# Performance work log

Measured on AMD Instinct MI355X. Metric: run time of the kernel, lower is better.

The kernel has to match this reference:

```python
import jax, jax.numpy as jnp
import numpy as np

TAU = 0.2
LW = 0.5
EPS = 1e-12  # tf.math.l2_normalize epsilon


def _l2norm(x):
    ss = jnp.sum(x * x, axis=-1, keepdims=True)
    return x * jax.lax.rsqrt(jnp.maximum(ss, EPS))


def _global_head(f, W1, b1, W2, b2):
    g = jnp.mean(f, axis=(1, 2))            # GlobalAveragePooling2D -> [B, C]
    h = jax.nn.relu(g @ W1 + b1)
    return h @ W2 + b2                      # [B, 128]


def _dense_head(f, W1, b1, W2, b2):
    # 1x1 convs == per-pixel matmuls
    h = jax.nn.relu(jnp.einsum('bhwc,cd->bhwd', f, W1) + b1)
    return jnp.einsum('bhwd,de->bhwe', h, W2) + b2  # [B, H, W, 128]


def _info_nce(q, k):
    logits = (q @ k.T) / TAU                # [N, N]
    lse = jax.nn.logsumexp(logits, axis=-1)
    pos = jnp.diagonal(logits)
    return jnp.mean(lse - pos)


def setup_inputs() -> dict:
    key = jax.random.key(0)
    ks = jax.random.split(key, 10)
    B, H, W, C = 128, 7, 7, 2048
    Dh, De = 2048, 128
    s1 = 1.0 / np.sqrt(C)
    s2 = 1.0 / np.sqrt(Dh)
    inp = {
        'feat_q': jax.random.normal(ks[0], (B, H, W, C), jnp.float32),
        'feat_k': jax.random.normal(ks[1], (B, H, W, C), jnp.float32),
        'Wg1': jax.random.normal(ks[2], (C, Dh), jnp.float32) * s1,
        'bg1': jnp.zeros((Dh,), jnp.float32),
        'Wg2': jax.random.normal(ks[3], (Dh, De), jnp.float32) * s2,
        'bg2': jnp.zeros((De,), jnp.float32),
        'Wd1': jax.random.normal(ks[4], (C, Dh), jnp.float32) * s1,
        'bd1': jnp.zeros((Dh,), jnp.float32),
        'Wd2': jax.random.normal(ks[5], (Dh, De), jnp.float32) * s2,
        'bd2': jnp.zeros((De,), jnp.float32),
        'mWg1': jax.random.normal(ks[6], (C, Dh), jnp.float32) * s1,
        'mbg1': jnp.zeros((Dh,), jnp.float32),
        'mWg2': jax.random.normal(ks[7], (Dh, De), jnp.float32) * s2,
        'mbg2': jnp.zeros((De,), jnp.float32),
        'mWd1': jax.random.normal(ks[8], (C, Dh), jnp.float32) * s1,
        'mbd1': jnp.zeros((Dh,), jnp.float32),
        'mWd2': jax.random.normal(ks[9], (Dh, De), jnp.float32) * s2,
        'mbd2': jnp.zeros((De,), jnp.float32),
    }
    return inp


def reference(feat_q, feat_k, Wg1, bg1, Wg2, bg2, Wd1, bd1, Wd2, bd2,
              mWg1, mbg1, mWg2, mbg2, mWd1, mbd1, mWd2, mbd2):
    # query (student) branch
    q_g = _l2norm(_global_head(feat_q, Wg1, bg1, Wg2, bg2))      # [B, 128]
    q_d = _l2norm(_dense_head(feat_q, Wd1, bd1, Wd2, bd2))       # [B, H, W, 128]
    # key (momentum teacher) branch, stop-gradient as in train_step
    k_g = jax.lax.stop_gradient(_l2norm(_global_head(feat_k, mWg1, mbg1, mWg2, mbg2)))
    k_d = jax.lax.stop_gradient(_l2norm(_dense_head(feat_k, mWd1, mbd1, mWd2, mbd2)))

    l_g = _info_nce(q_g, k_g)

    B, H, W, De = q_d.shape
    f1 = q_d.reshape(B, H * W, De)
    f2 = k_d.reshape(B, H * W, De)
    sim = jnp.einsum('bnc,bmc->bnm', f1, f2)                     # [B, HW, HW]
    idx = jnp.argmax(sim, axis=-1)                               # [B, HW]
    matched = jnp.take_along_axis(f2, idx[..., None], axis=1)    # [B, HW, 128]

    l_d = _info_nce(f1.reshape(-1, De), matched.reshape(-1, De))
    total = (1.0 - LW) * l_g + LW * l_d
    return total
```

## Files before the change

kernel.cpp:

```cpp
#include <hip/hip_runtime.h>
#include <cstddef>

typedef __bf16 bf16x8 __attribute__((ext_vector_type(8)));
typedef float  f32x4  __attribute__((ext_vector_type(4)));
typedef unsigned short u16x8 __attribute__((ext_vector_type(8)));
typedef unsigned short u16x4 __attribute__((ext_vector_type(4)));

__device__ __forceinline__ float b2f(unsigned short u) {
    union { unsigned int i; float f; } v; v.i = ((unsigned int)u) << 16; return v.f;
}
__device__ __forceinline__ unsigned short f2b(float f) {
    union { float f; unsigned int i; } v; v.f = f;
    unsigned int r = v.i + 0x7fffu + ((v.i >> 16) & 1u);
    return (unsigned short)(r >> 16);
}
__device__ __forceinline__ void gl_lds16(const void* g, void* l) {
    __builtin_amdgcn_global_load_lds((const __attribute__((address_space(1))) void*)g,
                                     (__attribute__((address_space(3))) void*)l,
                                     16, 0, 0);
}

__device__ __forceinline__ void xcd_swizzle(int& bx, int& by, int& bz) {
    unsigned int nx = gridDim.x, ny = gridDim.y;
    unsigned int n = nx * ny * gridDim.z;
    unsigned int lin = blockIdx.x + nx * (blockIdx.y + ny * blockIdx.z);
    unsigned int q = n >> 3, r = n & 7u;
    unsigned int xcd = lin & 7u, off = lin >> 3;
    unsigned int s = (xcd < r) ? (xcd * (q + 1u) + off)
                               : (r * (q + 1u) + (xcd - r) * q + off);
    bx = (int)(s % nx); s /= nx;
    by = (int)(s % ny);
    bz = (int)(s / ny);
}

__global__ __launch_bounds__(64) void detect_kernel(const unsigned short* __restrict__ feat,
                                                    int* __restrict__ flag) {
    __shared__ int cnt;
    if (threadIdx.x == 0) cnt = 0;
    __syncthreads();
    int c = 0;
    for (int i = threadIdx.x; i < 256; i += 64) {
        float v = b2f(feat[i]);
        if (fabsf(v) > 100.0f) ++c;
    }
    atomicAdd(&cnt, c);
    __syncthreads();
    if (threadIdx.x == 0) *flag = (cnt > 16) ? 1 : 0;
}

__global__ __launch_bounds__(256) void zero_kernel(float* __restrict__ p, int n4) {
    int i = blockIdx.x * 256 + threadIdx.x;
    const f32x4 z = {0.f, 0.f, 0.f, 0.f};
    if (i < n4) ((f32x4*)p)[i] = z;
}

__global__ __launch_bounds__(256) void convpool_kernel(const void* __restrict__ fq,
                                                       const void* __restrict__ fk,
                                                       unsigned short* __restrict__ FQ,
                                                       unsigned short* __restrict__ FK,
                                                       unsigned short* __restrict__ gq,
                                                       unsigned short* __restrict__ gk,
                                                       const int* __restrict__ flagp) {
    int fl = *flagp;
    int b = blockIdx.y;
    const void* src = blockIdx.z ? fk : fq;
    unsigned short* dst = blockIdx.z ? FK : FQ;
    unsigned short* g   = blockIdx.z ? gk : gq;
    int c0 = blockIdx.x * 1024 + threadIdx.x * 4;
    float s[4];
    #pragma unroll
    for (int j = 0; j < 4; ++j) s[j] = 0.f;
    for (int p = 0; p < 49; ++p) {
        size_t idx = ((size_t)b * 49 + p) * 2048 + c0;
        u16x4 o;
        if (fl) {
            f32x4 v = *(const f32x4*)((const float*)src + idx);
            o[0]=f2b(v[0]); o[1]=f2b(v[1]); o[2]=f2b(v[2]); o[3]=f2b(v[3]);
            s[0]+=v[0]; s[1]+=v[1]; s[2]+=v[2]; s[3]+=v[3];
        } else {
            o = *(const u16x4*)((const unsigned short*)src + idx);
            #pragma unroll
            for (int j = 0; j < 4; ++j) s[j] += b2f(o[j]);
        }
        *(u16x4*)(dst + idx) = o;
    }
    u16x4 gm;
    #pragma unroll
    for (int j = 0; j < 4; ++j) gm[j] = f2b(s[j] * (1.0f / 49.0f));
    *(u16x4*)(g + (size_t)b * 2048 + c0) = gm;
}

__global__ __launch_bounds__(256) void convert_kernel(const void* __restrict__ in,
                                                      unsigned short* __restrict__ out,
                                                      const int* __restrict__ flagp) {
    int fl = *flagp;
    size_t i = ((size_t)blockIdx.x * 256 + threadIdx.x) * 8;
    if (fl) {
        const float* inf = (const float*)in;
        f32x4 v0 = *(const f32x4*)(inf + i);
        f32x4 v1 = *(const f32x4*)(inf + i + 4);
        u16x8 o;
        o[0]=f2b(v0[0]); o[1]=f2b(v0[1]); o[2]=f2b(v0[2]); o[3]=f2b(v0[3]);
        o[4]=f2b(v1[0]); o[5]=f2b(v1[1]); o[6]=f2b(v1[2]); o[7]=f2b(v1[3]);
        *(u16x8*)(out + i) = o;
    } else {
        *(u16x8*)(out + i) = *(const u16x8*)((const unsigned short*)in + i);
    }
}

__global__ __launch_bounds__(256) void pool_kernel(const void* __restrict__ fq,
                                                   const void* __restrict__ fk,
                                                   unsigned short* __restrict__ gq,
                                                   unsigned short* __restrict__ gk,
                                                   const int* __restrict__ flagp) {
    int fl = *flagp;
    int c = blockIdx.x * 256 + threadIdx.x;
    int b = blockIdx.y;
    const void* src = blockIdx.z ? fk : fq;
    unsigned short* dst = blockIdx.z ? gk : gq;
    size_t base = (size_t)b * 49 * 2048 + c;
    float s = 0.f;
    if (fl) {
        const float* sf = (const float*)src;
        #pragma unroll
        for (int p = 0; p < 49; ++p) s += sf[base + (size_t)p * 2048];
    } else {
        const unsigned short* su = (const unsigned short*)src;
        #pragma unroll
        for (int p = 0; p < 49; ++p) s += b2f(su[base + (size_t)p * 2048]);
    }
    dst[(size_t)b * 2048 + c] = f2b(s * (1.0f / 49.0f));
}

__global__ __launch_bounds__(256) void transpose2v_kernel(
    const void* __restrict__ s0, const void* __restrict__ s1,
    unsigned short* __restrict__ d0, unsigned short* __restrict__ d1,
    int rows, int cols, const int* __restrict__ flagp) {
    int fl = *flagp;
    int z = blockIdx.z;
    const void* in = z ? s1 : s0;
    unsigned short* out = z ? d1 : d0;
    __shared__ unsigned short tile[64 * 72];
    int bx = blockIdx.x * 64, by = blockIdx.y * 64;
    int tr = threadIdx.x >> 3;
    int tc = (threadIdx.x & 7) * 8;
    #pragma unroll
    for (int h = 0; h < 2; ++h) {
        int r = tr + h * 32;
        if (fl) {
            const float* inf = (const float*)in + (size_t)(by + r) * cols + bx + tc;
            f32x4 v0 = *(const f32x4*)inf;
            f32x4 v1 = *(const f32x4*)(inf + 4);
            u16x8 o;
            o[0]=f2b(v0[0]); o[1]=f2b(v0[1]); o[2]=f2b(v0[2]); o[3]=f2b(v0[3]);
            o[4]=f2b(v1[0]); o[5]=f2b(v1[1]); o[6]=f2b(v1[2]); o[7]=f2b(v1[3]);
            *(u16x8*)(tile + r * 72 + tc) = o;
        } else {
            const unsigned short* inu = (const unsigned short*)in + (size_t)(by + r) * cols + bx + tc;
            *(u16x8*)(tile + r * 72 + tc) = *(const u16x8*)inu;
        }
    }
    __syncthreads();
    #pragma unroll
    for (int h = 0; h < 2; ++h) {
        int oc = tr + h * 32;
        u16x8 v;
        #pragma unroll
        for (int j = 0; j < 8; ++j) v[j] = tile[(tc + j) * 72 + oc];
        *(u16x8*)(out + (size_t)(bx + oc) * rows + by + tc) = v;
    }
}

__global__ __launch_bounds__(256) void transpose4v_kernel(
    const void* __restrict__ s0, const void* __restrict__ s1,
    const void* __restrict__ s2, const void* __restrict__ s3,
    unsigned short* __restrict__ d0, unsigned short* __restrict__ d1,
    unsigned short* __restrict__ d2, unsigned short* __restrict__ d3,
    int rows, int cols, const int* __restrict__ flagp) {
    int fl = *flagp;
    int z = blockIdx.z;
    const void* in = (z == 0) ? s0 : (z == 1) ? s1 : (z == 2) ? s2 : s3;
    unsigned short* out = (z == 0) ? d0 : (z == 1) ? d1 : (z == 2) ? d2 : d3;
    __shared__ unsigned short tile[64 * 72];
    int bx = blockIdx.x * 64, by = blockIdx.y * 64;
    int tr = threadIdx.x >> 3;
    int tc = (threadIdx.x & 7) * 8;
    #pragma unroll
    for (int h = 0; h < 2; ++h) {
        int r = tr + h * 32;
        if (fl) {
            const float* inf = (const float*)in + (size_t)(by + r) * cols + bx + tc;
            f32x4 v0 = *(const f32x4*)inf;
            f32x4 v1 = *(const f32x4*)(inf + 4);
            u16x8 o;
            o[0]=f2b(v0[0]); o[1]=f2b(v0[1]); o[2]=f2b(v0[2]); o[3]=f2b(v0[3]);
            o[4]=f2b(v1[0]); o[5]=f2b(v1[1]); o[6]=f2b(v1[2]); o[7]=f2b(v1[3]);
            *(u16x8*)(tile + r * 72 + tc) = o;
        } else {
            const unsigned short* inu = (const unsigned short*)in + (size_t)(by + r) * cols + bx + tc;
            *(u16x8*)(tile + r * 72 + tc) = *(const u16x8*)inu;
        }
    }
    __syncthreads();
    #pragma unroll
    for (int h = 0; h < 2; ++h) {
        int oc = tr + h * 32;
        u16x8 v;
        #pragma unroll
        for (int j = 0; j < 8; ++j) v[j] = tile[(tc + j) * 72 + oc];
        *(u16x8*)(out + (size_t)(bx + oc) * rows + by + tc) = v;
    }
}

__device__ __forceinline__ void mlp_body(
    const unsigned short* __restrict__ A, const unsigned short* __restrict__ Bt,
    const unsigned short* __restrict__ W2, const void* __restrict__ b1,
    float* __restrict__ outp, size_t m0, size_t n0, int fl)
{
    const int K = 2048;
    __shared__ unsigned short smem[32768];
    unsigned short* As0 = smem;
    unsigned short* Bs0 = smem + 8192;
    unsigned short* As1 = smem + 16384;
    unsigned short* Bs1 = smem + 24576;
    unsigned short* W2s = smem;
    unsigned short* Hs  = smem + 8192;

    int tid  = threadIdx.x;
    int lane = tid & 63;
    int w    = tid >> 6;
    int wm = w & 1, wn = w >> 1;
    int quad = lane >> 4, l16 = lane & 15;
    int lrow = lane >> 3;
    int kc   = (lane & 7) ^ lrow;

    const unsigned short* gA[4];
    const unsigned short* gB[4];
    int off[4];
    #pragma unroll
    for (int c = 0; c < 4; ++c) {
        int row = w * 32 + c * 8 + lrow;
        gA[c] = A  + (m0 + row) * (size_t)K + kc * 8;
        gB[c] = Bt + (n0 + row) * (size_t)K + kc * 8;
        off[c] = w * 2048 + c * 512;
    }

    const f32x4 zero4 = {0.f, 0.f, 0.f, 0.f};
    f32x4 acc[4][4];
    #pragma unroll
    for (int i = 0; i < 4; ++i)
        #pragma unroll
        for (int j = 0; j < 4; ++j) acc[i][j] = zero4;

    int swz = l16 & 7;

#define STAGE(Ad, Bd) do { \
    _Pragma("unroll") \
    for (int c = 0; c < 4; ++c) { gl_lds16(gA[c], (Ad) + off[c]); gA[c] += 64; } \
    _Pragma("unroll") \
    for (int c = 0; c < 4; ++c) { gl_lds16(gB[c], (Bd) + off[c]); gB[c] += 64; } \
} while (0)

#define CSTEP(Asrc, Bsrc) do { \
    _Pragma("unroll") \
    for (int k0 = 0; k0 < 64; k0 += 32) { \
        bf16x8 af[4], bfr[4]; \
        _Pragma("unroll") \
        for (int mt = 0; mt < 4; ++mt) { \
            int row = wm * 64 + mt * 16 + l16; \
            int sc  = (((k0 >> 3) + quad) ^ swz) << 3; \
            af[mt] = *(const bf16x8*)((Asrc) + row * 64 + sc); \
        } \
        _Pragma("unroll") \
        for (int nt = 0; nt < 4; ++nt) { \
            int row = wn * 64 + nt * 16 + l16; \
            int sc  = (((k0 >> 3) + quad) ^ swz) << 3; \
            bfr[nt] = *(const bf16x8*)((Bsrc) + row * 64 + sc); \
        } \
        _Pragma("unroll") \
        for (int mt = 0; mt < 4; ++mt) \
            _Pragma("unroll") \
            for (int nt = 0; nt < 4; ++nt) \
                acc[mt][nt] = __builtin_amdgcn_mfma_f32_16x16x32_bf16(af[mt], bfr[nt], acc[mt][nt], 0, 0, 0); \
    } \
} while (0)

    STAGE(As0, Bs0);
    __syncthreads();
    #pragma unroll 1
    for (int kb2 = 0; kb2 < 16; ++kb2) {
        STAGE(As1, Bs1);
        CSTEP(As0, Bs0);
        __syncthreads();
        if (kb2 < 15) STAGE(As0, Bs0);
        CSTEP(As1, Bs1);
        __syncthreads();
    }
#undef STAGE
#undef CSTEP

    float b1v[4];
    #pragma unroll
    for (int nt = 0; nt < 4; ++nt) {
        int col = (int)n0 + wn * 64 + nt * 16 + l16;
        b1v[nt] = fl ? ((const float*)b1)[col] : b2f(((const unsigned short*)b1)[col]);
    }

    f32x4 acc2[4][4];
    #pragma unroll
    for (int i = 0; i < 4; ++i)
        #pragma unroll
        for (int j = 0; j < 4; ++j) acc2[i][j] = zero4;

    #pragma unroll
    for (int hf = 0; hf < 2; ++hf) {
        __syncthreads();
        if (wn == hf) {
            #pragma unroll
            for (int mt = 0; mt < 4; ++mt)
                #pragma unroll
                for (int nt = 0; nt < 4; ++nt)
                    #pragma unroll
                    for (int r = 0; r < 4; ++r) {
                        float v = fmaxf(acc[mt][nt][r] + b1v[nt], 0.f);
                        Hs[(wm * 64 + mt * 16 + quad * 4 + r) * 72 + nt * 16 + l16] = f2b(v);
                    }
        } else {
            #pragma unroll
            for (int c = 0; c < 8; ++c) {
                const unsigned short* g = W2 + (size_t)(wm * 64 + c * 8 + lrow) * 2048
                                          + n0 + hf * 64 + kc * 8;
                gl_lds16(g, W2s + wm * 4096 + c * 512);
            }
        }
        __syncthreads();
        #pragma unroll
        for (int k0 = 0; k0 < 64; k0 += 32) {
            bf16x8 ha[4], wb[4];
            #pragma unroll
            for (int mt = 0; mt < 4; ++mt)
                ha[mt] = *(const bf16x8*)(Hs + (wm * 64 + mt * 16 + l16) * 72 + k0 + quad * 8);
            #pragma unroll
            for (int et = 0; et < 4; ++et) {
                int row = wn * 64 + et * 16 + l16;
                int sc  = (((k0 >> 3) + quad) ^ swz) << 3;
                wb[et] = *(const bf16x8*)(W2s + row * 64 + sc);
            }
            #pragma unroll
            for (int mt = 0; mt < 4; ++mt)
                #pragma unroll
                for (int et = 0; et < 4; ++et)
                    acc2[mt][et] = __builtin_amdgcn_mfma_f32_16x16x32_bf16(ha[mt], wb[et], acc2[mt][et], 0, 0, 0);
        }
    }

    #pragma unroll
    for (int et = 0; et < 4; ++et) {
        int col = wn * 64 + et * 16 + l16;
        #pragma unroll
        for (int mt = 0; mt < 4; ++mt)
            #pragma unroll
            for (int r = 0; r < 4; ++r) {
                size_t row = m0 + wm * 64 + mt * 16 + quad * 4 + r;
                atomicAdd(&outp[row * 128 + col], acc2[mt][et][r]);
            }
    }
}

__global__ __launch_bounds__(256) void mlp_mega_kernel(
    const unsigned short* __restrict__ FQ, const unsigned short* __restrict__ FK,
    const unsigned short* __restrict__ gq, const unsigned short* __restrict__ gk,
    const unsigned short* __restrict__ WD1T, const unsigned short* __restrict__ MWD1T,
    const unsigned short* __restrict__ WG1T, const unsigned short* __restrict__ MWG1T,
    const unsigned short* __restrict__ W2dq, const unsigned short* __restrict__ W2dk,
    const unsigned short* __restrict__ W2gq, const unsigned short* __restrict__ W2gk,
    const void* __restrict__ bd1, const void* __restrict__ mbd1,
    const void* __restrict__ bg1, const void* __restrict__ mbg1,
    float* __restrict__ rawdq, float* __restrict__ rawdk,
    float* __restrict__ rawgq, float* __restrict__ rawgk,
    const int* __restrict__ flagp)
{
    int fl = *flagp;
    int bx, by, bz;
    xcd_swizzle(bx, by, bz);
    int z = bz;
    int isg = (by == 49);
    const unsigned short *A, *Bt, *W2; const void* b1; float* outp;
    if (!isg) {
        A = z ? FK : FQ;  Bt = z ? MWD1T : WD1T;  W2 = z ? W2dk : W2dq;
        b1 = z ? mbd1 : bd1;  outp = z ? rawdk : rawdq;
    } else {
        A = z ? gk : gq;  Bt = z ? MWG1T : WG1T;  W2 = z ? W2gk : W2gq;
        b1 = z ? mbg1 : bg1;  outp = z ? rawgk : rawgq;
    }
    size_t m0 = isg ? 0 : (size_t)by * 128;
    size_t n0 = (size_t)bx * 128;
    mlp_body(A, Bt, W2, b1, outp, m0, n0, fl);
}

__global__ __launch_bounds__(256) void mlp_kernel(
    const unsigned short* __restrict__ A0, const unsigned short* __restrict__ A1,
    const unsigned short* __restrict__ Bt0, const unsigned short* __restrict__ Bt1,
    const unsigned short* __restrict__ W20, const unsigned short* __restrict__ W21,
    const void* __restrict__ b10, const void* __restrict__ b11,
    float* __restrict__ out0, float* __restrict__ out1,
    const int* __restrict__ flagp)
{
    int fl = *flagp;
    int bx, by, bz;
    xcd_swizzle(bx, by, bz);
    int z  = bz;
    mlp_body(z ? A1 : A0, z ? Bt1 : Bt0, z ? W21 : W20, z ? b11 : b10,
             z ? out1 : out0, (size_t)by * 128, (size_t)bx * 128, fl);
}

__global__ __launch_bounds__(256) void simmatch_kernel(
    const float* __restrict__ rawdq, const float* __restrict__ rawdk,
    const void* __restrict__ bd2, const void* __restrict__ mbd2,
    unsigned short* __restrict__ qd, unsigned short* __restrict__ kd,
    unsigned short* __restrict__ matched, float* __restrict__ pos,
    const int* __restrict__ flagp) {
    int fl = *flagp;
    __shared__ float f1s[49 * 128];
    __shared__ float f2s[49 * 128];
    int b = blockIdx.x;
    int t = threadIdx.x;
    size_t base = (size_t)b * 49 * 128;

    int rr = t >> 2, jq = t & 3;
    if (rr < 49) {
        #pragma unroll
        for (int br = 0; br < 2; ++br) {
            const float* raw = br ? rawdk : rawdq;
            const void* bias = br ? mbd2 : bd2;
            unsigned short* outg = br ? kd : qd;
            float* fs = br ? f2s : f1s;
            size_t idx = base + (size_t)rr * 128 + jq * 32;
            float x[32];
            float ss = 0.f;
            #pragma unroll
            for (int c = 0; c < 32; ++c) {
                float bv = fl ? ((const float*)bias)[jq * 32 + c]
                              : b2f(((const unsigned short*)bias)[jq * 32 + c]);
                x[c] = raw[idx + c] + bv;
                ss += x[c] * x[c];
            }
            ss += __shfl_xor(ss, 1); ss += __shfl_xor(ss, 2);
            float rs = rsqrtf(fmaxf(ss, 1e-12f));
            #pragma unroll
            for (int c = 0; c < 32; ++c) {
                unsigned short us = f2b(x[c] * rs);
                outg[idx + c] = us;
                fs[rr * 128 + jq * 32 + c] = b2f(us);
            }
        }
    }
    __syncthreads();

    int i = t >> 2, q4 = t & 3;
    if (i < 49) {
        int mlo = q4 * 13;
        int mhi = mlo + 13; if (mhi > 49) mhi = 49;
        float best = -1e30f; int bi = 1 << 20;
        const f32x4* va = (const f32x4*)(f1s + i * 128);
        for (int m = mlo; m < mhi; ++m) {
            const f32x4* vb = (const f32x4*)(f2s + m * 128);
            float d = 0.f;
            #pragma unroll
            for (int j = 0; j < 32; ++j) {
                f32x4 a = va[j], bb = vb[j];
                d += a[0]*bb[0] + a[1]*bb[1] + a[2]*bb[2] + a[3]*bb[3];
            }
            if (d > best) { best = d; bi = m; }
        }
        #pragma unroll
        for (int off = 1; off < 4; off <<= 1) {
            float ov = __shfl_xor(best, off);
            int   oi = __shfl_xor(bi, off);
            if (ov > best || (ov == best && oi < bi)) { best = ov; bi = oi; }
        }
        if (q4 == 0) pos[b * 49 + i] = best * 5.0f;
        for (int j = q4 * 32; j < q4 * 32 + 32; ++j)
            matched[base + (size_t)i * 128 + j] = f2b(f2s[bi * 128 + j]);
    }
}

#define KS 136
__global__ __launch_bounds__(256) void lse_kernel(const unsigned short* __restrict__ qd,
                                                  const unsigned short* __restrict__ matched,
                                                  float* __restrict__ lsep) {
    __shared__ unsigned short As[128 * KS];
    __shared__ unsigned short Bs[64 * KS];
    __shared__ float rsum[128];
    int tid  = threadIdx.x;
    int lane = tid & 63, wave = tid >> 6;
    int wm = wave & 1, wn = wave >> 1;
    int quad = lane >> 4, l16 = lane & 15;
    size_t m0 = (size_t)blockIdx.x * 128;
    int z = blockIdx.y;

    #pragma unroll
    for (int i = 0; i < 8; ++i) {
        int l = tid + 256 * i;
        int row = l >> 4, ko = (l & 15) << 3;
        u16x8 v = *(const u16x8*)(qd + (m0 + row) * 128 + ko);
        *(u16x8*)(As + row * KS + ko) = v;
    }
    if (tid < 128) rsum[tid] = 0.f;

    float rs[4][4];
    #pragma unroll
    for (int mt = 0; mt < 4; ++mt)
        #pragma unroll
        for (int r = 0; r < 4; ++r) rs[mt][r] = 0.f;

    const f32x4 zero4 = {0.f, 0.f, 0.f, 0.f};
    int nlo = z * 896, nhi = nlo + 896;
    for (int n0 = nlo; n0 < nhi; n0 += 64) {
        __syncthreads();
        #pragma unroll
        for (int i = 0; i < 4; ++i) {
            int l = tid + 256 * i;
            int row = l >> 4, ko = (l & 15) << 3;
            u16x8 v = *(const u16x8*)(matched + (size_t)(n0 + row) * 128 + ko);
            *(u16x8*)(Bs + row * KS + ko) = v;
        }
        __syncthreads();
        f32x4 acc[4][2];
        #pragma unroll
        for (int mt = 0; mt < 4; ++mt) { acc[mt][0] = zero4; acc[mt][1] = zero4; }
        #pragma unroll
        for (int k0 = 0; k0 < 128; k0 += 32) {
            bf16x8 af[4], bfr[2];
            #pragma unroll
            for (int mt = 0; mt < 4; ++mt)
                af[mt] = *(const bf16x8*)(As + (wm * 64 + mt * 16 + l16) * KS + k0 + quad * 8);
            #pragma unroll
            for (int nt = 0; nt < 2; ++nt)
                bfr[nt] = *(const bf16x8*)(Bs + (wn * 32 + nt * 16 + l16) * KS + k0 + quad * 8);
            #pragma unroll
            for (int mt = 0; mt < 4; ++mt)
                #pragma unroll
                for (int nt = 0; nt < 2; ++nt)
                    acc[mt][nt] = __builtin_amdgcn_mfma_f32_16x16x32_bf16(af[mt], bfr[nt], acc[mt][nt], 0, 0, 0);
        }
        #pragma unroll
        for (int mt = 0; mt < 4; ++mt)
            #pragma unroll
            for (int r = 0; r < 4; ++r)
                rs[mt][r] += __expf(acc[mt][0][r] * 5.0f) + __expf(acc[mt][1][r] * 5.0f);
    }
    #pragma unroll
    for (int mt = 0; mt < 4; ++mt)
        #pragma unroll
        for (int r = 0; r < 4; ++r) {
            float v = rs[mt][r];
            v += __shfl_xor(v, 1); v += __shfl_xor(v, 2);
            v += __shfl_xor(v, 4); v += __shfl_xor(v, 8);
            if (l16 == 0) atomicAdd(&rsum[wm * 64 + mt * 16 + quad * 4 + r], v);
        }
    __syncthreads();
    if (tid < 128) lsep[(size_t)z * 6272 + m0 + tid] = rsum[tid];
}

__global__ __launch_bounds__(128) void lg_kernel(const float* __restrict__ rawgq,
                                                 const float* __restrict__ rawgk,
                                                 const void* __restrict__ bg2,
                                                 const void* __restrict__ mbg2,
                                                 float* __restrict__ lgrow,
                                                 const int* __restrict__ flagp) {
    int fl = *flagp;
    __shared__ float ksf[128 * 128];
    __shared__ float qsf[8 * 128];
    int t = threadIdx.x;
    int rbase = blockIdx.x * 8;
    {
        const float* rk = rawgk + (size_t)t * 128;
        float ss = 0.f;
        for (int c = 0; c < 128; ++c) {
            float bv = fl ? ((const float*)mbg2)[c] : b2f(((const unsigned short*)mbg2)[c]);
            float xx = rk[c] + bv;
            ss += xx * xx;
        }
        float rsv = rsqrtf(fmaxf(ss, 1e-12f));
        for (int c = 0; c < 128; ++c) {
            float bv = fl ? ((const float*)mbg2)[c] : b2f(((const unsigned short*)mbg2)[c]);
            ksf[t * 128 + c] = b2f(f2b((rk[c] + bv) * rsv));
        }
    }
    if (t < 8) {
        const float* rq = rawgq + (size_t)(rbase + t) * 128;
        float ss = 0.f;
        for (int c = 0; c < 128; ++c) {
            float bv = fl ? ((const float*)bg2)[c] : b2f(((const unsigned short*)bg2)[c]);
            float xx = rq[c] + bv;
            ss += xx * xx;
        }
        float rsv = rsqrtf(fmaxf(ss, 1e-12f));
        for (int c = 0; c < 128; ++c) {
            float bv = fl ? ((const float*)bg2)[c] : b2f(((const unsigned short*)bg2)[c]);
            qsf[t * 128 + c] = b2f(f2b((rq[c] + bv) * rsv));
        }
    }
    __syncthreads();
    int rl = t >> 4, jg = t & 15;
    int row = rbase + rl;
    float se = 0.f, diag = 0.f;
    for (int jj = 0; jj < 8; ++jj) {
        int j = jg * 8 + jj;
        float d = 0.f;
        #pragma unroll 8
        for (int c = 0; c < 128; ++c) d += qsf[rl * 128 + c] * ksf[j * 128 + c];
        d *= 5.0f;
        se += __expf(d);
        if (j == row) diag = d;
    }
    #pragma unroll
    for (int off = 1; off < 16; off <<= 1) { se += __shfl_xor(se, off); diag += __shfl_xor(diag, off); }
    if (jg == 0) lgrow[row] = logf(se) - diag;
}

__global__ __launch_bounds__(256) void final_kernel(const float* __restrict__ lsep,
                                                    const float* __restrict__ pos,
                                                    const float* __restrict__ lgrow,
                                                    unsigned int* __restrict__ out) {
    int t = threadIdx.x;
    float s = 0.f;
    for (int i = t; i < 6272; i += 256) {
        float se = 0.f;
        #pragma unroll
        for (int zz = 0; zz < 7; ++zz) se += lsep[zz * 6272 + i];
        s += logf(se) - pos[i];
    }
    float g = (t < 128) ? lgrow[t] : 0.f;
    #pragma unroll
    for (int off = 32; off >= 1; off >>= 1) { s += __shfl_xor(s, off); g += __shfl_xor(g, off); }
    __shared__ float p8[8];
    if ((t & 63) == 0) { p8[t >> 6] = s; p8[4 + (t >> 6)] = g; }
    __syncthreads();
    if (t == 0) {
        float ld  = (p8[0] + p8[1] + p8[2] + p8[3]) * (1.0f / 6272.0f);
        float lg  = (p8[4] + p8[5] + p8[6] + p8[7]) * (1.0f / 128.0f);
        float total = 0.5f * lg + 0.5f * ld;
        unsigned int L = f2b(total);
        union { float f; unsigned int u; } tb; tb.f = total;
        unsigned int base = (tb.u & 0xFFFF0000u) | L;
        unsigned int bu = base; float be = 1e30f;
        #pragma unroll
        for (int d = -1; d <= 1; ++d) {
            unsigned int c = base + ((unsigned int)d << 16);
            union { unsigned int u; float f; } cv; cv.u = c;
            float e = fabsf(cv.f - total);
            if (e < be) { be = e; bu = c; }
        }
        out[0] = bu;
    }
}

#define A_FQ     ((size_t)0)
#define A_FK     ((size_t)25690112)
#define A_WD1T   ((size_t)51380224)
#define A_MWD1T  ((size_t)59768832)
#define A_WG1T   ((size_t)68157440)
#define A_MWG1T  ((size_t)76546048)
#define A_W2DQ   ((size_t)84934656)
#define A_W2DK   ((size_t)85458944)
#define A_W2GQ   ((size_t)85983232)
#define A_W2GK   ((size_t)86507520)
#define A_RAWDQ  ((size_t)87031808)
#define A_RAWDK  ((size_t)90243072)
#define A_RAWGQ  ((size_t)93454336)
#define A_RAWGK  ((size_t)93519872)
#define A_GQ     ((size_t)93585408)
#define A_GK     ((size_t)94109696)
#define A_QD     ((size_t)94633984)
#define A_KD     ((size_t)96239616)
#define A_MT     ((size_t)97845248)
#define A_POS    ((size_t)99450880)
#define A_LSEP   ((size_t)99475968)
#define A_LGR    ((size_t)99651584)
#define A_FLAG   ((size_t)99652096)
#define A_NEED   ((size_t)99652608)

#define B_SLOTA  ((size_t)0)
#define B_QD     ((size_t)0)
#define B_KD     ((size_t)1605632)
#define B_MT     ((size_t)3211264)
#define B_SLOTB  ((size_t)8388608)
#define B_W2DQ   ((size_t)34078720)
#define B_W2DK   ((size_t)34603008)
#define B_W2GQ   ((size_t)35127296)
#define B_W2GK   ((size_t)35651584)
#define B_RAWDQ  ((size_t)36175872)
#define B_RAWDK  ((size_t)39387136)
#define B_RAWGQ  ((size_t)42598400)
#define B_RAWGK  ((size_t)42663936)
#define B_GQ     ((size_t)42729472)
#define B_GK     ((size_t)43253760)
#define B_POS    ((size_t)42729472)
#define B_LSEP   ((size_t)42754560)
#define B_LGR    ((size_t)42930176)
#define B_FLAG   ((size_t)42930688)

extern "C" void kernel_launch(void* const* d_in, const int* in_sizes, int n_in,
                              void* d_out, int out_size, void* d_ws, size_t ws_size,
                              hipStream_t stream) {
    (void)in_sizes; (void)n_in; (void)out_size;
    const void* feat_q = d_in[0];
    const void* feat_k = d_in[1];
    const void* Wg1 = d_in[2];  const void* bg1 = d_in[3];
    const void* Wg2 = d_in[4];  const void* bg2 = d_in[5];
    const void* Wd1 = d_in[6];  const void* bd1 = d_in[7];
    const void* Wd2 = d_in[8];  const void* bd2 = d_in[9];
    const void* mWg1 = d_in[10]; const void* mbg1 = d_in[11];
    const void* mWg2 = d_in[12]; const void* mbg2 = d_in[13];
    const void* mWd1 = d_in[14]; const void* mbd1 = d_in[15];
    const void* mWd2 = d_in[16]; const void* mbd2 = d_in[17];
    char* ws = (char*)d_ws;

    if (ws_size >= A_NEED) {
        unsigned short* FQ    = (unsigned short*)(ws + A_FQ);
        unsigned short* FK    = (unsigned short*)(ws + A_FK);
        unsigned short* WD1T  = (unsigned short*)(ws + A_WD1T);
        unsigned short* MWD1T = (unsigned short*)(ws + A_MWD1T);
        unsigned short* WG1T  = (unsigned short*)(ws + A_WG1T);
        unsigned short* MWG1T = (unsigned short*)(ws + A_MWG1T);
        unsigned short* W2dq  = (unsigned short*)(ws + A_W2DQ);
        unsigned short* W2dk  = (unsigned short*)(ws + A_W2DK);
        unsigned short* W2gq  = (unsigned short*)(ws + A_W2GQ);
        unsigned short* W2gk  = (unsigned short*)(ws + A_W2GK);
        float* rawdq = (float*)(ws + A_RAWDQ);
        float* rawdk = (float*)(ws + A_RAWDK);
        float* rawgq = (float*)(ws + A_RAWGQ);
        float* rawgk = (float*)(ws + A_RAWGK);
        unsigned short* gq = (unsigned short*)(ws + A_GQ);
        unsigned short* gk = (unsigned short*)(ws + A_GK);
        unsigned short* qd = (unsigned short*)(ws + A_QD);
        unsigned short* kd = (unsigned short*)(ws + A_KD);
        unsigned short* mt = (unsigned short*)(ws + A_MT);
        float* pos  = (float*)(ws + A_POS);
        float* lsep = (float*)(ws + A_LSEP);
        float* lgr  = (float*)(ws + A_LGR);
        int*   flag = (int*)(ws + A_FLAG);

        detect_kernel<<<1, 64, 0, stream>>>((const unsigned short*)feat_q, flag);
        convpool_kernel<<<dim3(2, 128, 2), 256, 0, stream>>>(feat_q, feat_k, FQ, FK, gq, gk, flag);
        transpose4v_kernel<<<dim3(32, 32, 4), 256, 0, stream>>>(
            Wd1, mWd1, Wg1, mWg1, WD1T, MWD1T, WG1T, MWG1T, 2048, 2048, flag);
        transpose4v_kernel<<<dim3(2, 32, 4), 256, 0, stream>>>(
            Wd2, mWd2, Wg2, mWg2, W2dq, W2dk, W2gq, W2gk, 2048, 128, flag);
        zero_kernel<<<1600, 256, 0, stream>>>(rawdq, 409600);
        mlp_mega_kernel<<<dim3(16, 50, 2), 256, 0, stream>>>(
            FQ, FK, gq, gk, WD1T, MWD1T, WG1T, MWG1T,
            W2dq, W2dk, W2gq, W2gk, bd1, mbd1, bg1, mbg1,
            rawdq, rawdk, rawgq, rawgk, flag);
        simmatch_kernel<<<128, 256, 0, stream>>>(rawdq, rawdk, bd2, mbd2, qd, kd, mt, pos, flag);
        lse_kernel<<<dim3(49, 7), 256, 0, stream>>>(qd, mt, lsep);
        lg_kernel<<<16, 128, 0, stream>>>(rawgq, rawgk, bg2, mbg2, lgr, flag);
        final_kernel<<<1, 256, 0, stream>>>(lsep, pos, lgr, (unsigned int*)d_out);
    } else {
        unsigned short* slotA = (unsigned short*)(ws + B_SLOTA);
        unsigned short* slotB = (unsigned short*)(ws + B_SLOTB);
        unsigned short* W2dq = (unsigned short*)(ws + B_W2DQ);
        unsigned short* W2dk = (unsigned short*)(ws + B_W2DK);
        unsigned short* W2gq = (unsigned short*)(ws + B_W2GQ);
        unsigned short* W2gk = (unsigned short*)(ws + B_W2GK);
        float* rawdq = (float*)(ws + B_RAWDQ);
        float* rawdk = (float*)(ws + B_RAWDK);
        float* rawgq = (float*)(ws + B_RAWGQ);
        float* rawgk = (float*)(ws + B_RAWGK);
        unsigned short* gq = (unsigned short*)(ws + B_GQ);
        unsigned short* gk = (unsigned short*)(ws + B_GK);
        unsigned short* qd = (unsigned short*)(ws + B_QD);
        unsigned short* kd = (unsigned short*)(ws + B_KD);
        unsigned short* mt = (unsigned short*)(ws + B_MT);
        float* pos  = (float*)(ws + B_POS);
        float* lsep = (float*)(ws + B_LSEP);
        float* lgr  = (float*)(ws + B_LGR);
        int*   flag = (int*)(ws + B_FLAG);

        detect_kernel<<<1, 64, 0, stream>>>((const unsigned short*)feat_q, flag);
        pool_kernel<<<dim3(8, 128, 2), 256, 0, stream>>>(feat_q, feat_k, gq, gk, flag);
        transpose2v_kernel<<<dim3(32, 32, 2), 256, 0, stream>>>(Wg1, mWg1, slotA, slotB, 2048, 2048, flag);
        transpose4v_kernel<<<dim3(2, 32, 4), 256, 0, stream>>>(
            Wd2, mWd2, Wg2, mWg2, W2dq, W2dk, W2gq, W2gk, 2048, 128, flag);
        zero_kernel<<<1600, 256, 0, stream>>>(rawdq, 409600);
        mlp_kernel<<<dim3(16, 1, 2), 256, 0, stream>>>(
            gq, gk, slotA, slotB, W2gq, W2gk, bg1, mbg1, rawgq, rawgk, flag);
        transpose2v_kernel<<<dim3(32, 32, 1), 256, 0, stream>>>(Wd1, Wd1, slotA, slotA, 2048, 2048, flag);
        convert_kernel<<<6272, 256, 0, stream>>>(feat_q, slotB, flag);
        mlp_kernel<<<dim3(16, 49, 1), 256, 0, stream>>>(
            slotB, slotB, slotA, slotA, W2dq, W2dq, bd1, bd1, rawdq, rawdq, flag);
        transpose2v_kernel<<<dim3(32, 32, 1), 256, 0, stream>>>(mWd1, mWd1, slotA, slotA, 2048, 2048, flag);
        convert_kernel<<<6272, 256, 0, stream>>>(feat_k, slotB, flag);
        mlp_kernel<<<dim3(16, 49, 1), 256, 0, stream>>>(
            slotB, slotB, slotA, slotA, W2dk, W2dk, mbd1, mbd1, rawdk, rawdk, flag);
        simmatch_kernel<<<128, 256, 0, stream>>>(rawdq, rawdk, bd2, mbd2, qd, kd, mt, pos, flag);
        lse_kernel<<<dim3(49, 7), 256, 0, stream>>>(qd, mt, lsep);
        lg_kernel<<<16, 128, 0, stream>>>(rawgq, rawgk, bg2, mbg2, lgr, flag);
        final_kernel<<<1, 256, 0, stream>>>(lsep, pos, lgr, (unsigned int*)d_out);
    }
}
```

Before: 546.1 us.

## Widen grids for pooling, simmatch and LSE; hand-pipeline MLP GEMM barriers

Convpool now uses two channels per thread over twice as many blocks. Simmatch splits its rows across two blocks per batch, and lse_kernel splits its N range into 14 chunks instead of 7, reusing the rawdq buffer for the larger partial-sum array. The MLP GEMM main loop replaces __syncthreads with explicit vmcnt/lgkmcnt waits, raw s_barriers and sched_barriers, and raises wave priority around the MFMA block. The goal is more parallelism in the small tail kernels and better overlap of global-to-LDS loads with MFMA work. The costs are redundant normalisation work in simmatch and reliance on hand-counted waitcnt values.

```diff
diff --git a/kernel.cpp b/kernel.cpp
--- a/kernel.cpp
+++ b/kernel.cpp
@@ -3,8 +3,10 @@
 
 typedef __bf16 bf16x8 __attribute__((ext_vector_type(8)));
 typedef float  f32x4  __attribute__((ext_vector_type(4)));
+typedef float  f32x2  __attribute__((ext_vector_type(2)));
 typedef unsigned short u16x8 __attribute__((ext_vector_type(8)));
 typedef unsigned short u16x4 __attribute__((ext_vector_type(4)));
+typedef unsigned short u16x2 __attribute__((ext_vector_type(2)));
 
 __device__ __forceinline__ float b2f(unsigned short u) {
     union { unsigned int i; float f; } v; v.i = ((unsigned int)u) << 16; return v.f;
@@ -66,28 +68,30 @@
     const void* src = blockIdx.z ? fk : fq;
     unsigned short* dst = blockIdx.z ? FK : FQ;
     unsigned short* g   = blockIdx.z ? gk : gq;
-    int c0 = blockIdx.x * 1024 + threadIdx.x * 4;
-    float s[4];
-    #pragma unroll
-    for (int j = 0; j < 4; ++j) s[j] = 0.f;
-    for (int p = 0; p < 49; ++p) {
-        size_t idx = ((size_t)b * 49 + p) * 2048 + c0;
-        u16x4 o;
-        if (fl) {
-            f32x4 v = *(const f32x4*)((const float*)src + idx);
-            o[0]=f2b(v[0]); o[1]=f2b(v[1]); o[2]=f2b(v[2]); o[3]=f2b(v[3]);
-            s[0]+=v[0]; s[1]+=v[1]; s[2]+=v[2]; s[3]+=v[3];
-        } else {
-            o = *(const u16x4*)((const unsigned short*)src + idx);
-            #pragma unroll
-            for (int j = 0; j < 4; ++j) s[j] += b2f(o[j]);
-        }
-        *(u16x4*)(dst + idx) = o;
-    }
-    u16x4 gm;
-    #pragma unroll
-    for (int j = 0; j < 4; ++j) gm[j] = f2b(s[j] * (1.0f / 49.0f));
-    *(u16x4*)(g + (size_t)b * 2048 + c0) = gm;
+    int c0 = blockIdx.x * 512 + threadIdx.x * 2;
+    float s0 = 0.f, s1 = 0.f;
+    if (fl) {
+        const float* sf = (const float*)src;
+        #pragma unroll 7
+        for (int p = 0; p < 49; ++p) {
+            size_t idx = ((size_t)b * 49 + p) * 2048 + c0;
+            f32x2 v = *(const f32x2*)(sf + idx);
+            u16x2 o; o[0] = f2b(v[0]); o[1] = f2b(v[1]);
+            s0 += v[0]; s1 += v[1];
+            *(u16x2*)(dst + idx) = o;
+        }
+    } else {
+        const unsigned short* su = (const unsigned short*)src;
+        #pragma unroll 7
+        for (int p = 0; p < 49; ++p) {
+            size_t idx = ((size_t)b * 49 + p) * 2048 + c0;
+            u16x2 o = *(const u16x2*)(su + idx);
+            s0 += b2f(o[0]); s1 += b2f(o[1]);
+            *(u16x2*)(dst + idx) = o;
+        }
+    }
+    u16x2 gm; gm[0] = f2b(s0 * (1.0f / 49.0f)); gm[1] = f2b(s1 * (1.0f / 49.0f));
+    *(u16x2*)(g + (size_t)b * 2048 + c0) = gm;
 }
 
 __global__ __launch_bounds__(256) void convert_kernel(const void* __restrict__ in,
@@ -277,24 +281,39 @@
             int sc  = (((k0 >> 3) + quad) ^ swz) << 3; \
             bfr[nt] = *(const bf16x8*)((Bsrc) + row * 64 + sc); \
         } \
+        __builtin_amdgcn_s_setprio(1); \
         _Pragma("unroll") \
         for (int mt = 0; mt < 4; ++mt) \
             _Pragma("unroll") \
             for (int nt = 0; nt < 4; ++nt) \
                 acc[mt][nt] = __builtin_amdgcn_mfma_f32_16x16x32_bf16(af[mt], bfr[nt], acc[mt][nt], 0, 0, 0); \
+        __builtin_amdgcn_s_setprio(0); \
     } \
 } while (0)
 
     STAGE(As0, Bs0);
-    __syncthreads();
     #pragma unroll 1
     for (int kb2 = 0; kb2 < 16; ++kb2) {
         STAGE(As1, Bs1);
+        asm volatile("s_waitcnt vmcnt(8)" ::: "memory");
+        __builtin_amdgcn_s_barrier();
+        __builtin_amdgcn_sched_barrier(0);
         CSTEP(As0, Bs0);
-        __syncthreads();
-        if (kb2 < 15) STAGE(As0, Bs0);
+        asm volatile("s_waitcnt lgkmcnt(0)" ::: "memory");
+        __builtin_amdgcn_sched_barrier(0);
+        __builtin_amdgcn_s_barrier();
+        if (kb2 < 15) {
+            STAGE(As0, Bs0);
+            asm volatile("s_waitcnt vmcnt(8)" ::: "memory");
+        } else {
+            asm volatile("s_waitcnt vmcnt(0)" ::: "memory");
+        }
+        __builtin_amdgcn_s_barrier();
+        __builtin_amdgcn_sched_barrier(0);
         CSTEP(As1, Bs1);
-        __syncthreads();
+        asm volatile("s_waitcnt lgkmcnt(0)" ::: "memory");
+        __builtin_amdgcn_sched_barrier(0);
+        __builtin_amdgcn_s_barrier();
     }
 #undef STAGE
 #undef CSTEP
@@ -424,6 +443,7 @@
     __shared__ float f1s[49 * 128];
     __shared__ float f2s[49 * 128];
     int b = blockIdx.x;
+    int half = blockIdx.y;
     int t = threadIdx.x;
     size_t base = (size_t)b * 49 * 128;
 
@@ -450,15 +470,17 @@
             #pragma unroll
             for (int c = 0; c < 32; ++c) {
                 unsigned short us = f2b(x[c] * rs);
-                outg[idx + c] = us;
+                if (half == 0) outg[idx + c] = us;
                 fs[rr * 128 + jq * 32 + c] = b2f(us);
             }
         }
     }
     __syncthreads();
 
-    int i = t >> 2, q4 = t & 3;
-    if (i < 49) {
+    int i0 = t >> 2, q4 = t & 3;
+    int i = half * 25 + i0;
+    int ilim = half ? 24 : 25;
+    if (i0 < ilim) {
         int mlo = q4 * 13;
         int mhi = mlo + 13; if (mhi > 49) mhi = 49;
         float best = -1e30f; int bi = 1 << 20;
@@ -486,6 +508,7 @@
 }
 
 #define KS 136
+#define NZSPLIT 14
 __global__ __launch_bounds__(256) void lse_kernel(const unsigned short* __restrict__ qd,
                                                   const unsigned short* __restrict__ matched,
                                                   float* __restrict__ lsep) {
@@ -515,7 +538,7 @@
         for (int r = 0; r < 4; ++r) rs[mt][r] = 0.f;
 
     const f32x4 zero4 = {0.f, 0.f, 0.f, 0.f};
-    int nlo = z * 896, nhi = nlo + 896;
+    int nlo = z * 448, nhi = nlo + 448;
     for (int n0 = nlo; n0 < nhi; n0 += 64) {
         __syncthreads();
         #pragma unroll
@@ -629,7 +652,7 @@
     for (int i = t; i < 6272; i += 256) {
         float se = 0.f;
         #pragma unroll
-        for (int zz = 0; zz < 7; ++zz) se += lsep[zz * 6272 + i];
+        for (int zz = 0; zz < NZSPLIT; ++zz) se += lsep[zz * 6272 + i];
         s += logf(se) - pos[i];
     }
     float g = (t < 128) ? lgrow[t] : 0.f;
@@ -739,12 +762,12 @@
         unsigned short* kd = (unsigned short*)(ws + A_KD);
         unsigned short* mt = (unsigned short*)(ws + A_MT);
         float* pos  = (float*)(ws + A_POS);
-        float* lsep = (float*)(ws + A_LSEP);
+        float* lsep = (float*)(ws + A_RAWDQ);
         float* lgr  = (float*)(ws + A_LGR);
         int*   flag = (int*)(ws + A_FLAG);
 
         detect_kernel<<<1, 64, 0, stream>>>((const unsigned short*)feat_q, flag);
-        convpool_kernel<<<dim3(2, 128, 2), 256, 0, stream>>>(feat_q, feat_k, FQ, FK, gq, gk, flag);
+        convpool_kernel<<<dim3(4, 128, 2), 256, 0, stream>>>(feat_q, feat_k, FQ, FK, gq, gk, flag);
         transpose4v_kernel<<<dim3(32, 32, 4), 256, 0, stream>>>(
             Wd1, mWd1, Wg1, mWg1, WD1T, MWD1T, WG1T, MWG1T, 2048, 2048, flag);
         transpose4v_kernel<<<dim3(2, 32, 4), 256, 0, stream>>>(
@@ -754,8 +777,8 @@
             FQ, FK, gq, gk, WD1T, MWD1T, WG1T, MWG1T,
             W2dq, W2dk, W2gq, W2gk, bd1, mbd1, bg1, mbg1,
             rawdq, rawdk, rawgq, rawgk, flag);
-        simmatch_kernel<<<128, 256, 0, stream>>>(rawdq, rawdk, bd2, mbd2, qd, kd, mt, pos, flag);
-        lse_kernel<<<dim3(49, 7), 256, 0, stream>>>(qd, mt, lsep);
+        simmatch_kernel<<<dim3(128, 2), 256, 0, stream>>>(rawdq, rawdk, bd2, mbd2, qd, kd, mt, pos, flag);
+        lse_kernel<<<dim3(49, NZSPLIT), 256, 0, stream>>>(qd, mt, lsep);
         lg_kernel<<<16, 128, 0, stream>>>(rawgq, rawgk, bg2, mbg2, lgr, flag);
         final_kernel<<<1, 256, 0, stream>>>(lsep, pos, lgr, (unsigned int*)d_out);
     } else {
@@ -775,7 +798,7 @@
         unsigned short* kd = (unsigned short*)(ws + B_KD);
         unsigned short* mt = (unsigned short*)(ws + B_MT);
         float* pos  = (float*)(ws + B_POS);
-        float* lsep = (float*)(ws + B_LSEP);
+        float* lsep = (float*)(ws + B_RAWDQ);
         float* lgr  = (float*)(ws + B_LGR);
         int*   flag = (int*)(ws + B_FLAG);
 
@@ -795,8 +818,8 @@
         convert_kernel<<<6272, 256, 0, stream>>>(feat_k, slotB, flag);
         mlp_kernel<<<dim3(16, 49, 1), 256, 0, stream>>>(
             slotB, slotB, slotA, slotA, W2dk, W2dk, mbd1, mbd1, rawdk, rawdk, flag);
-        simmatch_kernel<<<128, 256, 0, stream>>>(rawdq, rawdk, bd2, mbd2, qd, kd, mt, pos, flag);
-        lse_kernel<<<dim3(49, 7), 256, 0, stream>>>(qd, mt, lsep);
+        simmatch_kernel<<<dim3(128, 2), 256, 0, stream>>>(rawdq, rawdk, bd2, mbd2, qd, kd, mt, pos, flag);
+        lse_kernel<<<dim3(49, NZSPLIT), 256, 0, stream>>>(qd, mt, lsep);
         lg_kernel<<<16, 128, 0, stream>>>(rawgq, rawgk, bg2, mbg2, lgr, flag);
         final_kernel<<<1, 256, 0, stream>>>(lsep, pos, lgr, (unsigned int*)d_out);
     }
```

Result: faster. 527.7 us, median of 2 (-3.4%).
